# Optimization experiments

Hardware: AMD Instinct MI355X
Metric: run time of the kernel (lower is better)

The kernel has to match this reference:

```python
import jax, jax.numpy as jnp
import numpy as np

B, L, D, H = 2, 2048, 1024, 16
DH = D // H
EPS = 1e-5


def setup_inputs() -> dict:
    key = jax.random.key(0)
    ks = jax.random.split(key, 8)
    s = 0.02  # realistic init scale for weights
    # causal mask: True where attention is DISALLOWED (masked_fill semantics)
    mask = jnp.triu(jnp.ones((L, L), dtype=bool), k=1)[None, None]  # [1,1,L,L]
    return {
        "x": jax.random.normal(ks[0], (B, L, D), jnp.float32),
        "mask": mask,
        "ln_g": jnp.ones((D,), jnp.float32),
        "ln_b": jnp.zeros((D,), jnp.float32),
        "Wq": jax.random.normal(ks[1], (D, D), jnp.float32) * s,
        "bq": jnp.zeros((D,), jnp.float32),
        "Wk": jax.random.normal(ks[2], (D, D), jnp.float32) * s,
        "bk": jnp.zeros((D,), jnp.float32),
        "Wv": jax.random.normal(ks[3], (D, D), jnp.float32) * s,
        "bv": jnp.zeros((D,), jnp.float32),
        "Wo": jax.random.normal(ks[4], (D, D), jnp.float32) * s,
        "bo": jnp.zeros((D,), jnp.float32),
    }


def _layernorm(x, g, b):
    mu = jnp.mean(x, axis=-1, keepdims=True)
    var = jnp.var(x, axis=-1, keepdims=True)
    return (x - mu) * jax.lax.rsqrt(var + EPS) * g + b


def reference(x, mask, ln_g, ln_b, Wq, bq, Wk, bk, Wv, bv, Wo, bo):
    b, l, d = x.shape
    h = _layernorm(x, ln_g, ln_b)
    # separate Q/K/V linears, split into heads: [b, H, l, DH]
    q = (h @ Wq + bq).reshape(b, l, H, DH).transpose(0, 2, 1, 3)
    k = (h @ Wk + bk).reshape(b, l, H, DH).transpose(0, 2, 1, 3)
    v = (h @ Wv + bv).reshape(b, l, H, DH).transpose(0, 2, 1, 3)
    scale = jnp.asarray(DH, x.dtype) ** -0.5
    # full L x L score matrix (this is exactly what the torch module does)
    w = jnp.einsum("bhqd,bhkd->bhqk", q, k) * scale
    w = jnp.where(mask, -jnp.inf, w)
    w = jax.nn.softmax(w, axis=-1)
    # dropout layers are identity in eval mode
    o = jnp.einsum("bhqk,bhkd->bhqd", w, v)
    o = o.transpose(0, 2, 1, 3).reshape(b, l, d)
    return o @ Wo + bo
```

## Files before the change

### kernel.cpp

```cpp
#include <hip/hip_runtime.h>
#include <hip/hip_bf16.h>


typedef __bf16  bf16x8 __attribute__((ext_vector_type(8)));
typedef __bf16  bf16x4 __attribute__((ext_vector_type(4)));
typedef float   f32x4  __attribute__((ext_vector_type(4)));
typedef float   f32x16 __attribute__((ext_vector_type(16)));

#define MFMA16(a, b, c) __builtin_amdgcn_mfma_f32_16x16x32_bf16(a, b, c, 0, 0, 0)
#define MFMA32(a, b, c) __builtin_amdgcn_mfma_f32_32x32x16_bf16(a, b, c, 0, 0, 0)

#define LDT 72
#define LDP 72
#define LDO 68

#define QSCALE 0.18033688011112042f

__device__ __forceinline__ void gl_lds16(const void* g, void* l) {
    __builtin_amdgcn_global_load_lds(
        (const __attribute__((address_space(1))) void*)g,
        (__attribute__((address_space(3))) void*)l, 16, 0, 0);
}

__global__ __launch_bounds__(256) void ln_kernel(
    const float* __restrict__ x, const float* __restrict__ g,
    const float* __restrict__ bta, __hip_bfloat16* __restrict__ h)
{
    __shared__ float red[8];
    const int row = blockIdx.x, t = threadIdx.x;
    const float* xr = x + (size_t)row * 1024;
    const float4 xv = *(const float4*)(xr + t * 4);
    float s  = xv.x + xv.y + xv.z + xv.w;
    float ss = xv.x * xv.x + xv.y * xv.y + xv.z * xv.z + xv.w * xv.w;
    #pragma unroll
    for (int off = 32; off > 0; off >>= 1) {
        s  += __shfl_down(s, off);
        ss += __shfl_down(ss, off);
    }
    const int lane = t & 63, wave = t >> 6;
    if (lane == 0) { red[wave] = s; red[4 + wave] = ss; }
    __syncthreads();
    const float S  = red[0] + red[1] + red[2] + red[3];
    const float SS = red[4] + red[5] + red[6] + red[7];
    const float mu   = S * (1.0f / 1024.0f);
    const float var  = SS * (1.0f / 1024.0f) - mu * mu;
    const float rstd = rsqrtf(var + 1e-5f);
    const float4 gv = *(const float4*)(g + t * 4);
    const float4 bv = *(const float4*)(bta + t * 4);
    bf16x4 hv;
    hv[0] = (__bf16)((xv.x - mu) * rstd * gv.x + bv.x);
    hv[1] = (__bf16)((xv.y - mu) * rstd * gv.y + bv.y);
    hv[2] = (__bf16)((xv.z - mu) * rstd * gv.z + bv.z);
    hv[3] = (__bf16)((xv.w - mu) * rstd * gv.w + bv.w);
    *(bf16x4*)(h + (size_t)row * 1024 + t * 4) = hv;
}

__global__ void transpose_cast_kernel(
    const float* __restrict__ Wq, const float* __restrict__ Wk,
    const float* __restrict__ Wv, const float* __restrict__ Wo,
    __hip_bfloat16* __restrict__ tq, __hip_bfloat16* __restrict__ tk,
    __hip_bfloat16* __restrict__ tv, __hip_bfloat16* __restrict__ to_)
{
    __shared__ float t[32][33];
    const int z = blockIdx.z;
    const float* src = (z == 0) ? Wq : (z == 1) ? Wk : (z == 2) ? Wv : Wo;
    __hip_bfloat16* dst = (z == 0) ? tq : (z == 1) ? tk : (z == 2) ? tv : to_;
    const int n0 = blockIdx.x * 32, k0 = blockIdx.y * 32;
    const int tx = threadIdx.x, ty = threadIdx.y;
    t[ty][tx] = src[(size_t)(k0 + ty) * 1024 + n0 + tx];
    __syncthreads();
    dst[(size_t)(n0 + ty) * 1024 + k0 + tx] = __float2bfloat16(t[tx][ty]);
}

__device__ __forceinline__ void gemm_core_1024(
    const __hip_bfloat16* __restrict__ A, const __hip_bfloat16* __restrict__ Bt,
    int m0, int n0, f32x4 (&acc)[4][2])
{
    __shared__ __align__(16) __hip_bfloat16 sA[128 * 64];
    __shared__ __align__(16) __hip_bfloat16 sB[128 * 64];
    const int tid  = threadIdx.x;
    const int wave = tid >> 6, lane = tid & 63;
    const int quad = lane >> 4, l16 = lane & 15;
    const int wm = wave >> 2, wn = wave & 3;

    const f32x4 zero = {0.f, 0.f, 0.f, 0.f};
    #pragma unroll
    for (int i = 0; i < 4; ++i)
        #pragma unroll
        for (int j = 0; j < 2; ++j) acc[i][j] = zero;

    const int r0 = tid >> 3;
    const int c0 = (((tid & 7) ^ (r0 & 7)) << 3);
    const __hip_bfloat16* Ap = A  + (size_t)(m0 + r0) * 1024 + c0;
    const __hip_bfloat16* Bp = Bt + (size_t)(n0 + r0) * 1024 + c0;
    __hip_bfloat16* lA0 = sA + tid * 8;
    __hip_bfloat16* lB0 = sB + tid * 8;

    const int rsw = l16 & 7;

    for (int k0 = 0; k0 < 1024; k0 += 64) {
        __syncthreads();
        gl_lds16(Ap + k0, lA0);
        gl_lds16(Ap + (size_t)64 * 1024 + k0, lA0 + 64 * 64);
        gl_lds16(Bp + k0, lB0);
        gl_lds16(Bp + (size_t)64 * 1024 + k0, lB0 + 64 * 64);
        __syncthreads();
        #pragma unroll
        for (int kk = 0; kk < 64; kk += 32) {
            const int sl = (((quad + (kk >> 3)) ^ rsw) << 3);
            bf16x8 af[4], bfr[2];
            #pragma unroll
            for (int mt = 0; mt < 4; ++mt)
                af[mt] = *(const bf16x8*)(sA + (wm * 64 + mt * 16 + l16) * 64 + sl);
            #pragma unroll
            for (int nt = 0; nt < 2; ++nt)
                bfr[nt] = *(const bf16x8*)(sB + (wn * 32 + nt * 16 + l16) * 64 + sl);
            #pragma unroll
            for (int mt = 0; mt < 4; ++mt)
                #pragma unroll
                for (int nt = 0; nt < 2; ++nt)
                    acc[mt][nt] = MFMA16(af[mt], bfr[nt], acc[mt][nt]);
        }
    }
}

__global__ __launch_bounds__(512) void gemm_qkv_kernel(
    const __hip_bfloat16* __restrict__ h,
    const __hip_bfloat16* __restrict__ wt_base,
    const float* __restrict__ bq, const float* __restrict__ bk,
    const float* __restrict__ bv,
    __hip_bfloat16* __restrict__ qkv_base)
{
    const int z = blockIdx.z;
    const __hip_bfloat16* wt = wt_base + ((size_t)z << 20);
    __hip_bfloat16* outp = qkv_base + ((size_t)z << 22);

    const bool swp = (z == 2);
    const __hip_bfloat16* A  = swp ? wt : h;
    const __hip_bfloat16* Bt = swp ? h  : wt;
    const int m0 = swp ? blockIdx.x * 128 : blockIdx.y * 128;
    const int n0 = swp ? blockIdx.y * 128 : blockIdx.x * 128;

    f32x4 acc[4][2];
    gemm_core_1024(A, Bt, m0, n0, acc);

    const int lane = threadIdx.x & 63, wave = threadIdx.x >> 6;
    const int quad = lane >> 4, l16 = lane & 15;
    const int wm = wave >> 2, wn = wave & 3;

    if (!swp) {
        const float* bias = (z == 0) ? bq : bk;
        const float scale = (z == 0) ? QSCALE : 1.0f;
        #pragma unroll
        for (int mt = 0; mt < 4; ++mt)
            #pragma unroll
            for (int nt = 0; nt < 2; ++nt)
                #pragma unroll
                for (int r = 0; r < 4; ++r) {
                    const int gm = m0 + wm * 64 + mt * 16 + quad * 4 + r;
                    const int gn = n0 + wn * 32 + nt * 16 + l16;
                    const float v = (acc[mt][nt][r] + bias[gn]) * scale;
                    const int b = gm >> 11, l = gm & 2047;
                    const int hh = gn >> 6, dh = gn & 63;
                    outp[(((((size_t)(b * 16 + hh)) << 11) + l) * 64) + dh] = __float2bfloat16(v);
                }
    } else {
        #pragma unroll
        for (int mt = 0; mt < 4; ++mt)
            #pragma unroll
            for (int nt = 0; nt < 2; ++nt)
                #pragma unroll
                for (int r = 0; r < 4; ++r) {
                    const int rr = m0 + wm * 64 + mt * 16 + quad * 4 + r;
                    const int cc = n0 + wn * 32 + nt * 16 + l16;
                    const float v = acc[mt][nt][r] + bv[rr];
                    const int b = cc >> 11, l = cc & 2047;
                    const int hh = rr >> 6, dh = rr & 63;
                    outp[((((size_t)(b * 16 + hh)) * 64 + dh) << 11) + l] = __float2bfloat16(v);
                }
    }
}

__global__ __launch_bounds__(512) void gemm_out_kernel(
    const __hip_bfloat16* __restrict__ o, const __hip_bfloat16* __restrict__ wot,
    const float* __restrict__ bo, float* __restrict__ out)
{
    __shared__ __align__(16) __hip_bfloat16 sA[64 * 64];
    __shared__ __align__(16) __hip_bfloat16 sB[128 * 64];
    const int tid  = threadIdx.x;
    const int wave = tid >> 6, lane = tid & 63;
    const int quad = lane >> 4, l16 = lane & 15;
    const int wm = wave >> 2, wn = wave & 3;
    const int m0 = blockIdx.y * 64, n0 = blockIdx.x * 128;

    const f32x4 zero = {0.f, 0.f, 0.f, 0.f};
    f32x4 acc[2][2];
    #pragma unroll
    for (int i = 0; i < 2; ++i)
        #pragma unroll
        for (int j = 0; j < 2; ++j) acc[i][j] = zero;

    const int r0 = tid >> 3;
    const int c0 = (((tid & 7) ^ (r0 & 7)) << 3);
    const __hip_bfloat16* Ap = o   + (size_t)(m0 + r0) * 1024 + c0;
    const __hip_bfloat16* Bp = wot + (size_t)(n0 + r0) * 1024 + c0;
    __hip_bfloat16* lA0 = sA + tid * 8;
    __hip_bfloat16* lB0 = sB + tid * 8;

    const int rsw = l16 & 7;

    for (int k0 = 0; k0 < 1024; k0 += 64) {
        __syncthreads();
        gl_lds16(Ap + k0, lA0);
        gl_lds16(Bp + k0, lB0);
        gl_lds16(Bp + (size_t)64 * 1024 + k0, lB0 + 64 * 64);
        __syncthreads();
        #pragma unroll
        for (int kk = 0; kk < 64; kk += 32) {
            const int sl = (((quad + (kk >> 3)) ^ rsw) << 3);
            bf16x8 af[2], bfr[2];
            #pragma unroll
            for (int mt = 0; mt < 2; ++mt)
                af[mt] = *(const bf16x8*)(sA + (wm * 32 + mt * 16 + l16) * 64 + sl);
            #pragma unroll
            for (int nt = 0; nt < 2; ++nt)
                bfr[nt] = *(const bf16x8*)(sB + (wn * 32 + nt * 16 + l16) * 64 + sl);
            #pragma unroll
            for (int mt = 0; mt < 2; ++mt)
                #pragma unroll
                for (int nt = 0; nt < 2; ++nt)
                    acc[mt][nt] = MFMA16(af[mt], bfr[nt], acc[mt][nt]);
        }
    }

    #pragma unroll
    for (int mt = 0; mt < 2; ++mt)
        #pragma unroll
        for (int nt = 0; nt < 2; ++nt)
            #pragma unroll
            for (int r = 0; r < 4; ++r) {
                const int gm = m0 + wm * 32 + mt * 16 + quad * 4 + r;
                const int gn = n0 + wn * 32 + nt * 16 + l16;
                out[(size_t)gm * 1024 + gn] = acc[mt][nt][r] + bo[gn];
            }
}

__global__ __launch_bounds__(512, 4) void attn_kernel(
    const __hip_bfloat16* __restrict__ Q,
    const __hip_bfloat16* __restrict__ Kg,
    const __hip_bfloat16* __restrict__ Vt,
    __hip_bfloat16* __restrict__ O)
{
    __shared__ __align__(16) char smem[55296];
    __hip_bfloat16* sK = (__hip_bfloat16*)smem;
    __hip_bfloat16* sV = (__hip_bfloat16*)(smem + 18432);
    __hip_bfloat16* sP = (__hip_bfloat16*)(smem + 36864);

    const int tid  = threadIdx.x;
    const int wave = tid >> 6, lane = tid & 63;
    const int grp  = wave >> 2, w4 = wave & 3;
    const int wk = w4 >> 1, wq = w4 & 1;
    const int q5 = lane & 31, hi = lane >> 5;
    const int bh = blockIdx.x, pi = blockIdx.y;
    const int qtA = 31 - pi, qtB = pi;
    const int q0A = qtA * 64, q0B = qtB * 64;

    const __hip_bfloat16* Qp = Q  + (size_t)bh * 2048 * 64;
    const __hip_bfloat16* Kp = Kg + (size_t)bh * 2048 * 64;
    const __hip_bfloat16* Vp = Vt + (size_t)bh * 64 * 2048;

    bf16x8 QfA[4], QfB[4];
    #pragma unroll
    for (int ks = 0; ks < 4; ++ks) {
        QfA[ks] = *(const bf16x8*)(Qp + (size_t)(q0A + wq * 32 + q5) * 64 + ks * 16 + hi * 8);
        QfB[ks] = *(const bf16x8*)(Qp + (size_t)(q0B + wq * 32 + q5) * 64 + ks * 16 + hi * 8);
    }

    f32x16 oA, oB;
    #pragma unroll
    for (int r = 0; r < 16; ++r) { oA[r] = 0.f; oB[r] = 0.f; }
    float lA = 0.f, lB = 0.f;

    const __hip_bfloat16* sKg = sK + grp * (64 * LDT);
    const __hip_bfloat16* sVg = sV + grp * (64 * LDT);
    __hip_bfloat16*       sPg = sP + grp * (64 * LDP);
    const int qloc = wq * 32 + q5;

    const int sg = tid >> 8, tt = tid & 255;

    auto phase1 = [&](const bf16x8 (&Qf)[4], float& l_run, bool diag) {
        f32x16 s;
        #pragma unroll
        for (int i = 0; i < 16; ++i) s[i] = 0.f;
        __builtin_amdgcn_s_setprio(1);
        #pragma unroll
        for (int ks = 0; ks < 4; ++ks) {
            const bf16x8 kf = *(const bf16x8*)(sKg + (wk * 32 + q5) * LDT + ks * 16 + hi * 8);
            s = MFMA32(kf, Qf[ks], s);
        }
        __builtin_amdgcn_s_setprio(0);
        if (diag) {
            #pragma unroll
            for (int i = 0; i < 16; ++i) {
                const int krow = wk * 32 + (i & 3) + 8 * (i >> 2) + 4 * hi;
                if (krow > qloc) s[i] = -1e30f;
            }
        }
        float rs = 0.f;
        #pragma unroll
        for (int rb = 0; rb < 4; ++rb) {
            bf16x4 pk;
            #pragma unroll
            for (int i = 0; i < 4; ++i) {
                const float p = exp2f(s[rb * 4 + i]);
                rs += p;
                pk[i] = (__bf16)p;
            }
            *(bf16x4*)(sPg + (wq * 32 + q5) * LDP + wk * 32 + 8 * rb + 4 * hi) = pk;
        }
        rs += __shfl_xor(rs, 32);
        l_run += rs;
    };
    auto phase2 = [&](f32x16& oacc) {
        __builtin_amdgcn_s_setprio(1);
        #pragma unroll
        for (int ks = 0; ks < 4; ++ks) {
            const bf16x8 vf = *(const bf16x8*)(sVg + (wk * 32 + q5) * LDT + ks * 16 + hi * 8);
            const bf16x8 pf = *(const bf16x8*)(sPg + (wq * 32 + q5) * LDP + ks * 16 + hi * 8);
            oacc = MFMA32(vf, pf, oacc);
        }
        __builtin_amdgcn_s_setprio(0);
    };

    for (int r = 0; r < 17; ++r) {
        __syncthreads();
        const int js = 2 * r + sg;
        if (js < 33) {
            const int ktS = (js <= qtA) ? js : js - qtA - 1;
            const int k0 = ktS * 64;
            __hip_bfloat16* dK = sK + sg * (64 * LDT);
            __hip_bfloat16* dV = sV + sg * (64 * LDT);
            #pragma unroll
            for (int i = 0; i < 2; ++i) {
                const int chunk = tt + 256 * i, rr = chunk >> 3, cc = (chunk & 7) << 3;
                *(int4*)(dK + rr * LDT + cc) = *(const int4*)(Kp + (size_t)(k0 + rr) * 64 + cc);
                *(int4*)(dV + rr * LDT + cc) = *(const int4*)(Vp + (size_t)rr * 2048 + k0 + cc);
            }
        }
        __syncthreads();

        const int j = 2 * r + grp;
        const bool act = (j < 33);
        const bool isA = act && (j <= qtA);
        if (act) {
            const int kt = isA ? j : j - qtA - 1;
            const bool diag = isA ? (kt == qtA) : (kt == qtB);
            if (isA) phase1(QfA, lA, diag);
            else     phase1(QfB, lB, diag);
        }
        __syncthreads();

        if (act) {
            if (isA) phase2(oA);
            else     phase2(oB);
        }
    }

    __syncthreads();
    float* Oscr = (float*)smem;
    float* lscr = (float*)(smem + 34816);

    if (grp == 1) {
        #pragma unroll
        for (int t2 = 0; t2 < 2; ++t2) {
            const f32x16& oc = t2 ? oB : oA;
            float* rowp = Oscr + (t2 * 64 + wq * 32 + q5) * LDO;
            #pragma unroll
            for (int rb = 0; rb < 4; ++rb) {
                f32x4 v = {oc[rb * 4 + 0], oc[rb * 4 + 1], oc[rb * 4 + 2], oc[rb * 4 + 3]};
                *(f32x4*)(rowp + wk * 32 + 8 * rb + 4 * hi) = v;
            }
        }
    }
    if (hi == 0) {
        lscr[((0 * 2 + grp) * 2 + wk) * 64 + wq * 32 + q5] = lA;
        lscr[((1 * 2 + grp) * 2 + wk) * 64 + wq * 32 + q5] = lB;
    }
    __syncthreads();
    if (grp == 0) {
        #pragma unroll
        for (int t2 = 0; t2 < 2; ++t2) {
            const f32x16& oc = t2 ? oB : oA;
            float* rowp = Oscr + (t2 * 64 + wq * 32 + q5) * LDO;
            #pragma unroll
            for (int rb = 0; rb < 4; ++rb) {
                float* p = rowp + wk * 32 + 8 * rb + 4 * hi;
                f32x4 v = *(const f32x4*)p;
                v[0] += oc[rb * 4 + 0]; v[1] += oc[rb * 4 + 1];
                v[2] += oc[rb * 4 + 2]; v[3] += oc[rb * 4 + 3];
                *(f32x4*)p = v;
            }
        }
    }
    __syncthreads();

    const int b = bh >> 4, hh = bh & 15;
    #pragma unroll
    for (int i = 0; i < 2; ++i) {
        const int chunk = tid + 512 * i;
        const int row = chunk >> 3, t2 = row >> 6, q = row & 63;
        const int col = (chunk & 7) << 3;
        const float lt = lscr[((t2 * 2 + 0) * 2 + 0) * 64 + q]
                       + lscr[((t2 * 2 + 0) * 2 + 1) * 64 + q]
                       + lscr[((t2 * 2 + 1) * 2 + 0) * 64 + q]
                       + lscr[((t2 * 2 + 1) * 2 + 1) * 64 + q];
        const float linv = 1.0f / lt;
        const float* src = Oscr + (t2 * 64 + q) * LDO + col;
        const f32x4 v0 = *(const f32x4*)src;
        const f32x4 v1 = *(const f32x4*)(src + 4);
        bf16x8 ov;
        ov[0] = (__bf16)(v0[0] * linv); ov[1] = (__bf16)(v0[1] * linv);
        ov[2] = (__bf16)(v0[2] * linv); ov[3] = (__bf16)(v0[3] * linv);
        ov[4] = (__bf16)(v1[0] * linv); ov[5] = (__bf16)(v1[1] * linv);
        ov[6] = (__bf16)(v1[2] * linv); ov[7] = (__bf16)(v1[3] * linv);
        const int q0X = t2 ? q0B : q0A;
        *(bf16x8*)(O + ((size_t)b * 2048 + q0X + q) * 1024 + hh * 64 + col) = ov;
    }
}

extern "C" void kernel_launch(void* const* d_in, const int* in_sizes, int n_in,
                              void* d_out, int out_size, void* d_ws, size_t ws_size,
                              hipStream_t stream) {
    const float* x    = (const float*)d_in[0];
    const float* ln_g = (const float*)d_in[2];
    const float* ln_b = (const float*)d_in[3];
    const float* Wq = (const float*)d_in[4];  const float* bq = (const float*)d_in[5];
    const float* Wk = (const float*)d_in[6];  const float* bk = (const float*)d_in[7];
    const float* Wv = (const float*)d_in[8];  const float* bv = (const float*)d_in[9];
    const float* Wo = (const float*)d_in[10]; const float* bo = (const float*)d_in[11];
    float* out = (float*)d_out;

    __hip_bfloat16* ws = (__hip_bfloat16*)d_ws;
    const size_t M1 = 1024 * 1024;
    __hip_bfloat16* h   = ws;
    __hip_bfloat16* wqt = ws + 4 * M1;
    __hip_bfloat16* wot = ws + 7 * M1;
    __hip_bfloat16* q   = ws + 8 * M1;
    __hip_bfloat16* k   = ws + 12 * M1;
    __hip_bfloat16* vt  = ws + 16 * M1;
    __hip_bfloat16* o   = h;

    ln_kernel<<<4096, 256, 0, stream>>>(x, ln_g, ln_b, h);
    transpose_cast_kernel<<<dim3(32, 32, 4), dim3(32, 32), 0, stream>>>(
        Wq, Wk, Wv, Wo, wqt, wqt + M1, wqt + 2 * M1, wot);
    gemm_qkv_kernel<<<dim3(8, 32, 3), 512, 0, stream>>>(h, wqt, bq, bk, bv, q);
    attn_kernel<<<dim3(32, 16), 512, 0, stream>>>(q, k, vt, o);
    gemm_out_kernel<<<dim3(8, 64), 512, 0, stream>>>(o, wot, bo, out);
}
```

Before: 191.4 us.

## Prefetch next K/V tile into registers and reload Q per tile

The global loads for the next K/V tile are issued into registers right after the current tile is written to shared memory, so their latency overlaps the current tile's QK and PV compute. The per-thread global-to-LDS address math is hoisted out of the loop. Q fragments are no longer held for the whole kernel but are reloaded from global memory at each phase1 call, freeing the registers needed for the staging buffers. The cost is an extra global Q read per tile and more live registers for the prefetch.

```diff
diff --git a/kernel.cpp b/kernel.cpp
--- a/kernel.cpp
+++ b/kernel.cpp
@@ -269,13 +269,6 @@
     const __hip_bfloat16* Kp = Kg + (size_t)bh * 2048 * 64;
     const __hip_bfloat16* Vp = Vt + (size_t)bh * 64 * 2048;
 
-    bf16x8 QfA[4], QfB[4];
-    #pragma unroll
-    for (int ks = 0; ks < 4; ++ks) {
-        QfA[ks] = *(const bf16x8*)(Qp + (size_t)(q0A + wq * 32 + q5) * 64 + ks * 16 + hi * 8);
-        QfB[ks] = *(const bf16x8*)(Qp + (size_t)(q0B + wq * 32 + q5) * 64 + ks * 16 + hi * 8);
-    }
-
     f32x16 oA, oB;
     #pragma unroll
     for (int r = 0; r < 16; ++r) { oA[r] = 0.f; oB[r] = 0.f; }
@@ -288,7 +281,37 @@
 
     const int sg = tid >> 8, tt = tid & 255;
 
-    auto phase1 = [&](const bf16x8 (&Qf)[4], float& l_run, bool diag) {
+    const int ch0 = tt,       rr0 = ch0 >> 3, cc0 = (ch0 & 7) << 3;
+    const int ch1 = tt + 256, rr1 = ch1 >> 3, cc1 = (ch1 & 7) << 3;
+    const __hip_bfloat16* Kb0 = Kp + (size_t)rr0 * 64 + cc0;
+    const __hip_bfloat16* Kb1 = Kp + (size_t)rr1 * 64 + cc1;
+    const __hip_bfloat16* Vb0 = Vp + (size_t)rr0 * 2048 + cc0;
+    const __hip_bfloat16* Vb1 = Vp + (size_t)rr1 * 2048 + cc1;
+    __hip_bfloat16* dK = sK + sg * (64 * LDT);
+    __hip_bfloat16* dV = sV + sg * (64 * LDT);
+    int4 kst0, kst1, vst0, vst1;
+
+    auto issue = [&](int js2) {
+        const int ktS = (js2 <= qtA) ? js2 : js2 - qtA - 1;
+        const int k0 = ktS * 64;
+        kst0 = *(const int4*)(Kb0 + (size_t)k0 * 64);
+        kst1 = *(const int4*)(Kb1 + (size_t)k0 * 64);
+        vst0 = *(const int4*)(Vb0 + k0);
+        vst1 = *(const int4*)(Vb1 + k0);
+    };
+    auto wr_stage = [&]() {
+        *(int4*)(dK + rr0 * LDT + cc0) = kst0;
+        *(int4*)(dK + rr1 * LDT + cc1) = kst1;
+        *(int4*)(dV + rr0 * LDT + cc0) = vst0;
+        *(int4*)(dV + rr1 * LDT + cc1) = vst1;
+    };
+
+    auto phase1 = [&](int q0, float& l_run, bool diag) {
+        const __hip_bfloat16* qp = Qp + (size_t)(q0 + wq * 32 + q5) * 64 + hi * 8;
+        bf16x8 Qf[4];
+        #pragma unroll
+        for (int ks = 0; ks < 4; ++ks)
+            Qf[ks] = *(const bf16x8*)(qp + ks * 16);
         f32x16 s;
         #pragma unroll
         for (int i = 0; i < 16; ++i) s[i] = 0.f;
@@ -332,21 +355,14 @@
         __builtin_amdgcn_s_setprio(0);
     };
 
+    issue(sg);
+
     for (int r = 0; r < 17; ++r) {
         __syncthreads();
         const int js = 2 * r + sg;
-        if (js < 33) {
-            const int ktS = (js <= qtA) ? js : js - qtA - 1;
-            const int k0 = ktS * 64;
-            __hip_bfloat16* dK = sK + sg * (64 * LDT);
-            __hip_bfloat16* dV = sV + sg * (64 * LDT);
-            #pragma unroll
-            for (int i = 0; i < 2; ++i) {
-                const int chunk = tt + 256 * i, rr = chunk >> 3, cc = (chunk & 7) << 3;
-                *(int4*)(dK + rr * LDT + cc) = *(const int4*)(Kp + (size_t)(k0 + rr) * 64 + cc);
-                *(int4*)(dV + rr * LDT + cc) = *(const int4*)(Vp + (size_t)rr * 2048 + k0 + cc);
-            }
-        }
+        if (js < 33) wr_stage();
+        const int jsn = js + 2;
+        if (jsn < 33) issue(jsn);
         __syncthreads();
 
         const int j = 2 * r + grp;
@@ -355,8 +371,8 @@
         if (act) {
             const int kt = isA ? j : j - qtA - 1;
             const bool diag = isA ? (kt == qtA) : (kt == qtB);
-            if (isA) phase1(QfA, lA, diag);
-            else     phase1(QfB, lB, diag);
+            if (isA) phase1(q0A, lA, diag);
+            else     phase1(q0B, lB, diag);
         }
         __syncthreads();
 
```

Result: slower. 203.8 us (+6.4%).
